# Kernel tuning notes

Hardware: AMD Instinct MI355X
Metric: run time of the kernel (lower is better)

## Reference

```python
import jax, jax.numpy as jnp
import numpy as np

B, S, D, V, ML = 8, 1024, 768, 32000, 2000
EPS = 1e-5


def layernorm(x, g, b):
    mu = jnp.mean(x, axis=-1, keepdims=True)
    var = jnp.mean(jnp.square(x - mu), axis=-1, keepdims=True)
    return (x - mu) * jax.lax.rsqrt(var + EPS) * g + b


def setup_inputs() -> dict:
    key = jax.random.key(0)
    ks = jax.random.split(key, 16)
    idx = jax.random.randint(ks[0], (B, S), 0, V)
    attention_mask = jax.random.randint(ks[1], (B, S), 0, 2).astype(jnp.int32)
    # guarantee at least one valid key per row so softmax rows are finite
    attention_mask = attention_mask.at[:, 0].set(1)
    s = 0.02
    return {
        "idx": idx,
        "attention_mask": attention_mask,
        "emb": jax.random.normal(ks[2], (V, D), jnp.float32) * s,
        "pos_emb": jax.random.normal(ks[3], (ML, D), jnp.float32) * s,
        "Wq": jax.random.normal(ks[4], (D, D), jnp.float32) * s,
        "Wk": jax.random.normal(ks[5], (D, D), jnp.float32) * s,
        "Wv": jax.random.normal(ks[6], (D, D), jnp.float32) * s,
        "ln1_g": jnp.ones((D,), jnp.float32),
        "ln1_b": jnp.zeros((D,), jnp.float32),
        "W1": jax.random.normal(ks[7], (D, D), jnp.float32) * s,
        "b1": jnp.zeros((D,), jnp.float32),
        "W2": jax.random.normal(ks[8], (D, D), jnp.float32) * s,
        "b2": jnp.zeros((D,), jnp.float32),
        "ln2_g": jnp.ones((D,), jnp.float32),
        "ln2_b": jnp.zeros((D,), jnp.float32),
    }


def reference(idx, attention_mask, emb, pos_emb, Wq, Wk, Wv, ln1_g, ln1_b,
              W1, b1, W2, b2, ln2_g, ln2_b):
    seq_len = idx.shape[1]
    x = emb[idx] + pos_emb[:seq_len]                       # [B,S,D]
    q = x @ Wq                                             # [B,S,D]
    k = x @ Wk
    v = x @ Wv
    att = jnp.einsum('bqd,bkd->bqk', q, k) * (D ** -0.5)   # [B,S,S]
    att = jnp.where(attention_mask[:, None, :] == 0, -jnp.inf, att)
    a = jax.nn.softmax(att, axis=-1) @ v                   # [B,S,D]
    x = layernorm(a, ln1_g, ln1_b)
    h = jax.nn.gelu(x @ W1 + b1, approximate=False)        # exact GELU (torch default)
    h = jax.nn.gelu(h @ W2 + b2, approximate=False)
    return layernorm(h, ln2_g, ln2_b)
```

## Files before the change

### kernel.cpp

```cpp
#include <hip/hip_runtime.h>
#include <hip/hip_bf16.h>
#include <math.h>

typedef __bf16 bf16;
typedef __attribute__((ext_vector_type(8))) __bf16 bf16x8;
typedef __attribute__((ext_vector_type(4))) __bf16 bf16x4;
typedef __attribute__((ext_vector_type(4))) float f32x4;

#define NB 8
#define SEQ 1024
#define DIM 768
#define ROWS (NB*SEQ)

__device__ __forceinline__ float gelu_exact(float x){
  return 0.5f * x * (1.0f + erff(x * 0.70710678118654752440f));
}

__device__ __forceinline__ void gload_lds16(const void* g, void* l){
  __builtin_amdgcn_global_load_lds((const __attribute__((address_space(1))) void*)g,
                                   (__attribute__((address_space(3))) void*)l, 16, 0, 0);
}

__global__ __launch_bounds__(192)
void k_embed(const int* __restrict__ idx, const float* __restrict__ emb,
             const float* __restrict__ pos, bf16* __restrict__ xo){
  const int row = blockIdx.x;
  const int s = row & (SEQ-1);
  const int tok = idx[row];
  const float* e = emb + (long)tok*DIM;
  const float* p = pos + (long)s*DIM;
  bf16* o = xo + (long)row*DIM;
  const int tid = threadIdx.x;
  f32x4 ev = *(const f32x4*)(e + tid*4);
  f32x4 pv = *(const f32x4*)(p + tid*4);
  bf16x4 ov;
  ov[0]=(bf16)(ev[0]+pv[0]); ov[1]=(bf16)(ev[1]+pv[1]);
  ov[2]=(bf16)(ev[2]+pv[2]); ov[3]=(bf16)(ev[3]+pv[3]);
  *(bf16x4*)(o + tid*4) = ov;
}

__global__ __launch_bounds__(256)
void k_transpose_bf16(const float* __restrict__ src, bf16* __restrict__ dst,
                      int K, int N){
  __shared__ float t[32][33];
  const int n0 = blockIdx.x*32, k0 = blockIdx.y*32;
  const int tx = threadIdx.x, ty = threadIdx.y;
  #pragma unroll
  for (int i=0;i<4;i++)
    t[ty+i*8][tx] = src[(long)(k0+ty+i*8)*N + n0 + tx];
  __syncthreads();
  #pragma unroll
  for (int i=0;i<4;i++)
    dst[(long)(n0+ty+i*8)*K + k0 + tx] = (bf16)t[tx][ty+i*8];
}

__global__ __launch_bounds__(256)
void k_transpose_v(const bf16* __restrict__ qkv, bf16* __restrict__ vT){
  __shared__ bf16 t[32][33];
  const int b = blockIdx.z;
  const int s0 = blockIdx.x*32, d0 = blockIdx.y*32;
  const int tx = threadIdx.x, ty = threadIdx.y;
  const bf16* src = qkv + (long)b*SEQ*2304 + 1536;
  bf16* dst = vT + (long)b*DIM*SEQ;
  #pragma unroll
  for (int i=0;i<4;i++)
    t[ty+i*8][tx] = src[(long)(s0+ty+i*8)*2304 + d0 + tx];
  __syncthreads();
  #pragma unroll
  for (int i=0;i<4;i++)
    dst[(long)(d0+ty+i*8)*SEQ + s0 + tx] = t[tx][ty+i*8];
}

template<int EPI>
__global__ __launch_bounds__(512, 2)
void k_gemm(const bf16* __restrict__ A, int lda, long sA,
            const bf16* __restrict__ Bt, int ldb, long sB,
            void* __restrict__ Cv, int ldc, long sC,
            int K,
            const float* __restrict__ bias,
            const int* __restrict__ mask, int maskStride,
            float scale, int swizzle)
{
  __shared__ __align__(16) bf16 As[2][256][64];
  __shared__ __align__(16) bf16 Bs[2][256][64];

  const int bz = blockIdx.z;
  A  += (long)bz * sA;
  Bt += (long)bz * sB;

  int bx = blockIdx.x, by = blockIdx.y;
  if (swizzle){
    const int gx = gridDim.x;
    const int T  = gx * gridDim.y;
    const int flat = by*gx + bx;
    const int logical = (flat & 7)*(T>>3) + (flat>>3);
    bx = logical % gx;
    by = logical / gx;
  }
  const int m0 = bx*256, n0 = by*256;

  const int tid  = threadIdx.x;
  const int lane = tid & 63;
  const int w    = tid >> 6;
  const int wm   = w >> 2;
  const int wn   = w & 3;
  const int hb   = wn >> 1;
  const int gb   = wm*2 + (wn & 1);
  const int ga   = wn;

  const int l8    = lane >> 3;
  const int lslot = (lane & 7) ^ l8;

  const bf16* Agbase = A  + (long)(m0 + wm*128)*lda + lslot*8;
  const bf16* Bgbase = Bt + (long)(n0 + hb*128)*ldb + lslot*8;

  auto stageA = [&](int buf, int kt, int c){
    const bf16* g = Agbase + (long)(c*8 + l8)*lda + kt*64;
    char* l = (char*)&As[buf][0][0] + wm*16384 + c*1024;
    gload_lds16(g, l);
  };
  auto stageB = [&](int buf, int kt, int c){
    const bf16* g = Bgbase + (long)(c*8 + l8)*ldb + kt*64;
    char* l = (char*)&Bs[buf][0][0] + hb*16384 + c*1024;
    gload_lds16(g, l);
  };
  auto ldsA = [&](int buf, int mf, int ks)->bf16x8 {
    const int row  = wm*128 + mf*16 + (lane & 15);
    const int slot = (ks*4 + (lane>>4)) ^ (row & 7);
    return *(const bf16x8*)((const char*)&As[buf][0][0] + row*128 + slot*16);
  };
  auto ldsB = [&](int buf, int nf, int ks)->bf16x8 {
    const int row  = wn*64 + nf*16 + (lane & 15);
    const int slot = (ks*4 + (lane>>4)) ^ (row & 7);
    return *(const bf16x8*)((const char*)&Bs[buf][0][0] + row*128 + slot*16);
  };

  f32x4 acc[8][4];
  const f32x4 zero = {0.f,0.f,0.f,0.f};
  #pragma unroll
  for (int i=0;i<8;i++)
    #pragma unroll
    for (int j=0;j<4;j++) acc[i][j] = zero;

  bf16x8 bfr[4][2];
  const int nk = K >> 6;

  stageB(0,0, gb);    stageB(0,0, gb+4);
  stageB(0,0, gb+8);  stageB(0,0, gb+12);
  stageA(0,0, ga);    stageA(0,0, ga+4);
  stageA(0,0, ga+8);  stageA(0,0, ga+12);
  asm volatile("s_waitcnt vmcnt(2)\ns_barrier" ::: "memory");

  for (int t=0; t<nk; ++t){
    const int buf = t & 1;
    const bool st = (t+1 < nk);
    #pragma unroll
    for (int q=0; q<4; ++q){
      bf16x8 afr[2][2];
      #pragma unroll
      for (int i=0;i<2;i++)
        #pragma unroll
        for (int ks=0;ks<2;ks++)
          afr[i][ks] = ldsA(buf, 2*q+i, ks);
      if (q==0){
        #pragma unroll
        for (int nf=0;nf<4;nf++)
          #pragma unroll
          for (int ks=0;ks<2;ks++)
            bfr[nf][ks] = ldsB(buf, nf, ks);
      }
      if (st){
        if (q==0){ stageB(buf^1, t+1, gb);    stageB(buf^1, t+1, gb+4);  }
        if (q==1){ stageB(buf^1, t+1, gb+8);  stageB(buf^1, t+1, gb+12); }
        if (q==2){ stageA(buf^1, t+1, ga);    stageA(buf^1, t+1, ga+4);  }
        if (q==3){ stageA(buf^1, t+1, ga+8);  stageA(buf^1, t+1, ga+12); }
      }
      if (st){
        if (q==3) asm volatile("s_waitcnt vmcnt(2)\ns_barrier" ::: "memory");
        else      asm volatile("s_waitcnt vmcnt(4)\ns_barrier" ::: "memory");
      } else {
        if (q==1) asm volatile("s_waitcnt vmcnt(0)\ns_barrier" ::: "memory");
        else      asm volatile("s_barrier" ::: "memory");
      }
      __builtin_amdgcn_s_setprio(1);
      #pragma unroll
      for (int i=0;i<2;i++)
        #pragma unroll
        for (int nf=0;nf<4;nf++)
          #pragma unroll
          for (int ks=0;ks<2;ks++)
            acc[2*q+i][nf] = __builtin_amdgcn_mfma_f32_16x16x32_bf16(
                afr[i][ks], bfr[nf][ks], acc[2*q+i][nf], 0, 0, 0);
      __builtin_amdgcn_s_setprio(0);
      asm volatile("s_barrier" ::: "memory");
    }
  }

  const int cm0 = m0 + wm*128 + ((lane>>4)<<2);
  const int cn0 = n0 + wn*64  + (lane & 15);
  const long cb = (long)bz * sC;
  const int* mk = (EPI==3) ? (mask + (long)bz*maskStride) : nullptr;

  #pragma unroll
  for (int mf=0; mf<8; mf++){
    #pragma unroll
    for (int nf=0; nf<4; nf++){
      #pragma unroll
      for (int r=0; r<4; r++){
        const int m = cm0 + mf*16 + r;
        const int n = cn0 + nf*16;
        const long o = cb + (long)m*ldc + n;
        float c = acc[mf][nf][r];
        if (EPI == 0){
          ((bf16*)Cv)[o] = (bf16)c;
        } else if (EPI == 1){
          ((bf16*)Cv)[o] = (bf16)gelu_exact(c + bias[n]);
        } else if (EPI == 2){
          ((float*)Cv)[o] = gelu_exact(c + bias[n]);
        } else if (EPI == 3){
          ((float*)Cv)[o] = (mk[n] != 0) ? c*scale : -1e30f;
        } else {
          ((float*)Cv)[o] = c;
        }
      }
    }
  }
}

__global__ __launch_bounds__(256)
void k_softmax(const float* __restrict__ att, bf16* __restrict__ P){
  __shared__ float red[4];
  __shared__ float red2[4];
  const int row = blockIdx.x;
  const float* a = att + (long)row * SEQ;
  bf16* p = P + (long)row * SEQ;
  const int tid = threadIdx.x;
  f32x4 v = *(const f32x4*)(a + tid*4);
  float m = fmaxf(fmaxf(v[0],v[1]), fmaxf(v[2],v[3]));
  #pragma unroll
  for (int o=32;o>0;o>>=1) m = fmaxf(m, __shfl_xor(m, o));
  if ((tid&63)==0) red[tid>>6] = m;
  __syncthreads();
  m = fmaxf(fmaxf(red[0],red[1]), fmaxf(red[2],red[3]));
  float e0 = expf(v[0]-m), e1 = expf(v[1]-m), e2 = expf(v[2]-m), e3 = expf(v[3]-m);
  float s = e0+e1+e2+e3;
  #pragma unroll
  for (int o=32;o>0;o>>=1) s += __shfl_xor(s, o);
  if ((tid&63)==0) red2[tid>>6] = s;
  __syncthreads();
  s = red2[0]+red2[1]+red2[2]+red2[3];
  const float inv = 1.0f / s;
  bf16x4 pw;
  pw[0]=(bf16)(e0*inv); pw[1]=(bf16)(e1*inv); pw[2]=(bf16)(e2*inv); pw[3]=(bf16)(e3*inv);
  *(bf16x4*)(p + tid*4) = pw;
}

template<int OUT_BF16>
__global__ __launch_bounds__(256)
void k_layernorm(const float* __restrict__ X, const float* __restrict__ g,
                 const float* __restrict__ b, void* __restrict__ Yv){
  __shared__ float red[4];
  __shared__ float red2[4];
  const int row = blockIdx.x;
  const float* x = X + (long)row*DIM;
  const int tid = threadIdx.x;
  float v0=x[tid], v1=x[tid+256], v2=x[tid+512];
  float s = v0+v1+v2;
  #pragma unroll
  for (int o=32;o>0;o>>=1) s += __shfl_xor(s, o);
  if ((tid&63)==0) red[tid>>6] = s;
  __syncthreads();
  s = red[0]+red[1]+red[2]+red[3];
  const float mu = s * (1.0f/768.0f);
  const float d0=v0-mu, d1=v1-mu, d2=v2-mu;
  float q = d0*d0+d1*d1+d2*d2;
  #pragma unroll
  for (int o=32;o>0;o>>=1) q += __shfl_xor(q, o);
  if ((tid&63)==0) red2[tid>>6] = q;
  __syncthreads();
  q = red2[0]+red2[1]+red2[2]+red2[3];
  const float r = rsqrtf(q*(1.0f/768.0f) + 1e-5f);
  const float y0 = d0*r*g[tid]     + b[tid];
  const float y1 = d1*r*g[tid+256] + b[tid+256];
  const float y2 = d2*r*g[tid+512] + b[tid+512];
  if (OUT_BF16){
    bf16* Y = (bf16*)Yv;
    Y[(long)row*DIM+tid]=(bf16)y0; Y[(long)row*DIM+tid+256]=(bf16)y1; Y[(long)row*DIM+tid+512]=(bf16)y2;
  } else {
    float* Y = (float*)Yv;
    Y[(long)row*DIM+tid]=y0; Y[(long)row*DIM+tid+256]=y1; Y[(long)row*DIM+tid+512]=y2;
  }
}

extern "C" void kernel_launch(void* const* d_in, const int* in_sizes, int n_in,
                              void* d_out, int out_size, void* d_ws, size_t ws_size,
                              hipStream_t stream)
{
  (void)in_sizes; (void)n_in; (void)out_size; (void)ws_size;
  const int*   idx  = (const int*)d_in[0];
  const int*   am   = (const int*)d_in[1];
  const float* emb  = (const float*)d_in[2];
  const float* pos  = (const float*)d_in[3];
  const float* Wq   = (const float*)d_in[4];
  const float* Wk   = (const float*)d_in[5];
  const float* Wv   = (const float*)d_in[6];
  const float* ln1g = (const float*)d_in[7];
  const float* ln1b = (const float*)d_in[8];
  const float* W1   = (const float*)d_in[9];
  const float* b1   = (const float*)d_in[10];
  const float* W2   = (const float*)d_in[11];
  const float* b2   = (const float*)d_in[12];
  const float* ln2g = (const float*)d_in[13];
  const float* ln2b = (const float*)d_in[14];

  char* ws = (char*)d_ws;
  size_t off = 0;
  auto take = [&](size_t bytes)->char*{
    char* p = ws + off;
    off += (bytes + 255) & ~(size_t)255;
    return p;
  };
  bf16*  Wqkvt = (bf16*) take((size_t)2304*768*2);
  bf16*  W1t   = (bf16*) take((size_t)768*768*2);
  bf16*  W2t   = (bf16*) take((size_t)768*768*2);
  bf16*  xbf   = (bf16*) take((size_t)ROWS*DIM*2);
  bf16*  qkv   = (bf16*) take((size_t)ROWS*2304*2);
  bf16*  vT    = (bf16*) take((size_t)NB*DIM*SEQ*2);
  float* att   = (float*)take((size_t)NB*SEQ*SEQ*4);
  bf16*  P     = (bf16*) take((size_t)NB*SEQ*SEQ*2);
  float* aout  = (float*)take((size_t)ROWS*DIM*4);
  bf16*  x1    = (bf16*) take((size_t)ROWS*DIM*2);
  bf16*  h1    = (bf16*) take((size_t)ROWS*DIM*2);
  float* h2    = (float*)take((size_t)ROWS*DIM*4);
  float* out   = (float*)d_out;

  const dim3 tb(32,8);
  const dim3 tg(24,24);
  k_transpose_bf16<<<tg, tb, 0, stream>>>(Wq, Wqkvt,            768, 768);
  k_transpose_bf16<<<tg, tb, 0, stream>>>(Wk, Wqkvt + 768*768,  768, 768);
  k_transpose_bf16<<<tg, tb, 0, stream>>>(Wv, Wqkvt + 1536*768, 768, 768);
  k_transpose_bf16<<<tg, tb, 0, stream>>>(W1, W1t, 768, 768);
  k_transpose_bf16<<<tg, tb, 0, stream>>>(W2, W2t, 768, 768);

  k_embed<<<ROWS, 192, 0, stream>>>(idx, emb, pos, xbf);

  k_gemm<0><<<dim3(32,9,1), 512, 0, stream>>>(xbf,768,0L, Wqkvt,768,0L,
                                              qkv,2304,0L, 768,
                                              nullptr, nullptr,0, 1.0f, 1);

  k_transpose_v<<<dim3(32,24,8), tb, 0, stream>>>(qkv, vT);

  k_gemm<3><<<dim3(4,4,8), 512, 0, stream>>>(
      qkv,     2304, (long)SEQ*2304,
      qkv+768, 2304, (long)SEQ*2304,
      att,     SEQ,  (long)SEQ*SEQ,
      768, nullptr, am, SEQ, 0.03608439182435161f, 0);

  k_softmax<<<ROWS, 256, 0, stream>>>(att, P);

  k_gemm<4><<<dim3(4,3,8), 512, 0, stream>>>(
      P,    SEQ, (long)SEQ*SEQ,
      vT,   SEQ, (long)DIM*SEQ,
      aout, DIM, (long)SEQ*DIM,
      1024, nullptr, nullptr,0, 1.0f, 0);

  k_layernorm<1><<<ROWS, 256, 0, stream>>>(aout, ln1g, ln1b, x1);

  k_gemm<1><<<dim3(32,3,1), 512, 0, stream>>>(x1,768,0L, W1t,768,0L, h1,768,0L,
                                              768, b1, nullptr,0, 1.0f, 1);
  k_gemm<2><<<dim3(32,3,1), 512, 0, stream>>>(h1,768,0L, W2t,768,0L, h2,768,0L,
                                              768, b2, nullptr,0, 1.0f, 1);

  k_layernorm<0><<<ROWS, 256, 0, stream>>>(h2, ln2g, ln2b, out);
}
```

Measured before the change: 403.8 us.

## Add smaller-tile GEMM for attention/MLP, store scores in bf16, merge weight transposes

Adds a 128x128 tile, 256-thread double-buffered GEMM and uses it for QK^T, PV and both MLP GEMMs. The QKV projection keeps the large 256x256 tile kernel. The goal is more blocks on undersized grids such as 4x4x8 and 4x3x8, which should fill more compute units. Attention scores are now written and read as bf16 instead of fp32, halving that traffic at some cost in precision. The five weight-transpose launches become one launch.

```diff
diff --git a/kernel.cpp b/kernel.cpp
--- a/kernel.cpp
+++ b/kernel.cpp
@@ -40,18 +40,23 @@
 }
 
 __global__ __launch_bounds__(256)
-void k_transpose_bf16(const float* __restrict__ src, bf16* __restrict__ dst,
-                      int K, int N){
+void k_transpose_w(const float* __restrict__ Wq, const float* __restrict__ Wk,
+                   const float* __restrict__ Wv, const float* __restrict__ W1,
+                   const float* __restrict__ W2,
+                   bf16* __restrict__ Wqkvt, bf16* __restrict__ W1t, bf16* __restrict__ W2t){
   __shared__ float t[32][33];
+  const int z = blockIdx.z;
+  const float* src = (z==0)?Wq:(z==1)?Wk:(z==2)?Wv:(z==3)?W1:W2;
+  bf16* dst = (z<3) ? (Wqkvt + (size_t)z*768*768) : ((z==3)?W1t:W2t);
   const int n0 = blockIdx.x*32, k0 = blockIdx.y*32;
   const int tx = threadIdx.x, ty = threadIdx.y;
   #pragma unroll
   for (int i=0;i<4;i++)
-    t[ty+i*8][tx] = src[(long)(k0+ty+i*8)*N + n0 + tx];
+    t[ty+i*8][tx] = src[(long)(k0+ty+i*8)*768 + n0 + tx];
   __syncthreads();
   #pragma unroll
   for (int i=0;i<4;i++)
-    dst[(long)(n0+ty+i*8)*K + k0 + tx] = (bf16)t[tx][ty+i*8];
+    dst[(long)(n0+ty+i*8)*768 + k0 + tx] = (bf16)t[tx][ty+i*8];
 }
 
 __global__ __launch_bounds__(256)
@@ -72,14 +77,118 @@
 }
 
 template<int EPI>
+__global__ __launch_bounds__(256, 2)
+void k_gemm2p(const bf16* __restrict__ A, int lda, long sA,
+              const bf16* __restrict__ Bt, int ldb, long sB,
+              void* __restrict__ Cv, int ldc, long sC,
+              int K,
+              const float* __restrict__ bias,
+              const int* __restrict__ mask, int maskStride,
+              float scale)
+{
+  __shared__ __align__(16) bf16 As[2][128][32];
+  __shared__ __align__(16) bf16 Bs[2][128][32];
+
+  const int bz = blockIdx.z;
+  A  += (long)bz * sA;
+  Bt += (long)bz * sB;
+  const int m0 = blockIdx.x * 128;
+  const int n0 = blockIdx.y * 128;
+
+  const int tid  = threadIdx.x;
+  const int lane = tid & 63;
+  const int w    = tid >> 6;
+
+  const int st_row = w*16 + (lane>>2);
+  const int st_col = (lane&3)*8;
+  const bf16* Ag0 = A  + (long)(m0 + st_row)*lda + st_col;
+  const bf16* Bg0 = Bt + (long)(n0 + st_row)*ldb + st_col;
+
+  const int nk = K >> 5;
+
+  f32x4 acc[4][4];
+  const f32x4 zero = {0.f,0.f,0.f,0.f};
+  #pragma unroll
+  for (int i=0;i<4;i++)
+    #pragma unroll
+    for (int j=0;j<4;j++) acc[i][j] = zero;
+
+  const int wr = (w>>1)*64;
+  const int wc = (w&1)*64;
+  const int fr = lane & 15;
+  const int fk = (lane>>4)*8;
+
+  {
+    char* lA = (char*)&As[0][0][0] + w*1024;
+    char* lB = (char*)&Bs[0][0][0] + w*1024;
+    gload_lds16(Ag0,                lA);
+    gload_lds16(Ag0 + (long)64*lda, lA + 4096);
+    gload_lds16(Bg0,                lB);
+    gload_lds16(Bg0 + (long)64*ldb, lB + 4096);
+  }
+
+  int buf = 0;
+  for (int kt=0; kt<nk; kt++){
+    __syncthreads();
+    if (kt+1 < nk){
+      const bf16* Ag = Ag0 + (kt+1)*32;
+      const bf16* Bg = Bg0 + (kt+1)*32;
+      char* lA = (char*)&As[buf^1][0][0] + w*1024;
+      char* lB = (char*)&Bs[buf^1][0][0] + w*1024;
+      gload_lds16(Ag,                lA);
+      gload_lds16(Ag + (long)64*lda, lA + 4096);
+      gload_lds16(Bg,                lB);
+      gload_lds16(Bg + (long)64*ldb, lB + 4096);
+    }
+    bf16x8 af[4], bfv[4];
+    #pragma unroll
+    for (int t=0;t<4;t++){
+      af[t]  = *(const bf16x8*)&As[buf][wr + t*16 + fr][fk];
+      bfv[t] = *(const bf16x8*)&Bs[buf][wc + t*16 + fr][fk];
+    }
+    #pragma unroll
+    for (int mt=0;mt<4;mt++)
+      #pragma unroll
+      for (int nt=0;nt<4;nt++)
+        acc[mt][nt] = __builtin_amdgcn_mfma_f32_16x16x32_bf16(af[mt], bfv[nt], acc[mt][nt], 0, 0, 0);
+    buf ^= 1;
+  }
+
+  const int cm0 = m0 + wr + ((lane>>4)<<2);
+  const int cn0 = n0 + wc + fr;
+  const long cb = (long)bz * sC;
+  const int* mk = (EPI==3) ? (mask + (long)bz*maskStride) : nullptr;
+
+  #pragma unroll
+  for (int mt=0;mt<4;mt++){
+    #pragma unroll
+    for (int nt=0;nt<4;nt++){
+      #pragma unroll
+      for (int r=0;r<4;r++){
+        const int m = cm0 + mt*16 + r;
+        const int n = cn0 + nt*16;
+        const long o = cb + (long)m*ldc + n;
+        float c = acc[mt][nt][r];
+        if (EPI == 1){
+          ((bf16*)Cv)[o] = (bf16)gelu_exact(c + bias[n]);
+        } else if (EPI == 2){
+          ((float*)Cv)[o] = gelu_exact(c + bias[n]);
+        } else if (EPI == 3){
+          ((bf16*)Cv)[o] = (bf16)((mk[n] != 0) ? c*scale : -1e30f);
+        } else {
+          ((float*)Cv)[o] = c;
+        }
+      }
+    }
+  }
+}
+
+template<int EPI>
 __global__ __launch_bounds__(512, 2)
-void k_gemm(const bf16* __restrict__ A, int lda, long sA,
-            const bf16* __restrict__ Bt, int ldb, long sB,
-            void* __restrict__ Cv, int ldc, long sC,
-            int K,
-            const float* __restrict__ bias,
-            const int* __restrict__ mask, int maskStride,
-            float scale, int swizzle)
+void k_gemm4p(const bf16* __restrict__ A, int lda, long sA,
+              const bf16* __restrict__ Bt, int ldb, long sB,
+              void* __restrict__ Cv, int ldc, long sC,
+              int K, int swizzle)
 {
   __shared__ __align__(16) bf16 As[2][256][64];
   __shared__ __align__(16) bf16 Bs[2][256][64];
@@ -199,7 +308,6 @@
   const int cm0 = m0 + wm*128 + ((lane>>4)<<2);
   const int cn0 = n0 + wn*64  + (lane & 15);
   const long cb = (long)bz * sC;
-  const int* mk = (EPI==3) ? (mask + (long)bz*maskStride) : nullptr;
 
   #pragma unroll
   for (int mf=0; mf<8; mf++){
@@ -210,39 +318,29 @@
         const int m = cm0 + mf*16 + r;
         const int n = cn0 + nf*16;
         const long o = cb + (long)m*ldc + n;
-        float c = acc[mf][nf][r];
-        if (EPI == 0){
-          ((bf16*)Cv)[o] = (bf16)c;
-        } else if (EPI == 1){
-          ((bf16*)Cv)[o] = (bf16)gelu_exact(c + bias[n]);
-        } else if (EPI == 2){
-          ((float*)Cv)[o] = gelu_exact(c + bias[n]);
-        } else if (EPI == 3){
-          ((float*)Cv)[o] = (mk[n] != 0) ? c*scale : -1e30f;
-        } else {
-          ((float*)Cv)[o] = c;
-        }
+        ((bf16*)Cv)[o] = (bf16)acc[mf][nf][r];
       }
     }
   }
 }
 
 __global__ __launch_bounds__(256)
-void k_softmax(const float* __restrict__ att, bf16* __restrict__ P){
+void k_softmax(const bf16* __restrict__ att, bf16* __restrict__ P){
   __shared__ float red[4];
   __shared__ float red2[4];
   const int row = blockIdx.x;
-  const float* a = att + (long)row * SEQ;
+  const bf16* a = att + (long)row * SEQ;
   bf16* p = P + (long)row * SEQ;
   const int tid = threadIdx.x;
-  f32x4 v = *(const f32x4*)(a + tid*4);
-  float m = fmaxf(fmaxf(v[0],v[1]), fmaxf(v[2],v[3]));
+  bf16x4 v4 = *(const bf16x4*)(a + tid*4);
+  float v0=(float)v4[0], v1=(float)v4[1], v2=(float)v4[2], v3=(float)v4[3];
+  float m = fmaxf(fmaxf(v0,v1), fmaxf(v2,v3));
   #pragma unroll
   for (int o=32;o>0;o>>=1) m = fmaxf(m, __shfl_xor(m, o));
   if ((tid&63)==0) red[tid>>6] = m;
   __syncthreads();
   m = fmaxf(fmaxf(red[0],red[1]), fmaxf(red[2],red[3]));
-  float e0 = expf(v[0]-m), e1 = expf(v[1]-m), e2 = expf(v[2]-m), e3 = expf(v[3]-m);
+  float e0 = expf(v0-m), e1 = expf(v1-m), e2 = expf(v2-m), e3 = expf(v3-m);
   float s = e0+e1+e2+e3;
   #pragma unroll
   for (int o=32;o>0;o>>=1) s += __shfl_xor(s, o);
@@ -326,7 +424,7 @@
   bf16*  xbf   = (bf16*) take((size_t)ROWS*DIM*2);
   bf16*  qkv   = (bf16*) take((size_t)ROWS*2304*2);
   bf16*  vT    = (bf16*) take((size_t)NB*DIM*SEQ*2);
-  float* att   = (float*)take((size_t)NB*SEQ*SEQ*4);
+  bf16*  att   = (bf16*) take((size_t)NB*SEQ*SEQ*2);
   bf16*  P     = (bf16*) take((size_t)NB*SEQ*SEQ*2);
   float* aout  = (float*)take((size_t)ROWS*DIM*4);
   bf16*  x1    = (bf16*) take((size_t)ROWS*DIM*2);
@@ -334,42 +432,35 @@
   float* h2    = (float*)take((size_t)ROWS*DIM*4);
   float* out   = (float*)d_out;
 
-  const dim3 tb(32,8);
-  const dim3 tg(24,24);
-  k_transpose_bf16<<<tg, tb, 0, stream>>>(Wq, Wqkvt,            768, 768);
-  k_transpose_bf16<<<tg, tb, 0, stream>>>(Wk, Wqkvt + 768*768,  768, 768);
-  k_transpose_bf16<<<tg, tb, 0, stream>>>(Wv, Wqkvt + 1536*768, 768, 768);
-  k_transpose_bf16<<<tg, tb, 0, stream>>>(W1, W1t, 768, 768);
-  k_transpose_bf16<<<tg, tb, 0, stream>>>(W2, W2t, 768, 768);
+  k_transpose_w<<<dim3(24,24,5), dim3(32,8), 0, stream>>>(Wq,Wk,Wv,W1,W2, Wqkvt,W1t,W2t);
 
   k_embed<<<ROWS, 192, 0, stream>>>(idx, emb, pos, xbf);
 
-  k_gemm<0><<<dim3(32,9,1), 512, 0, stream>>>(xbf,768,0L, Wqkvt,768,0L,
-                                              qkv,2304,0L, 768,
-                                              nullptr, nullptr,0, 1.0f, 1);
-
-  k_transpose_v<<<dim3(32,24,8), tb, 0, stream>>>(qkv, vT);
-
-  k_gemm<3><<<dim3(4,4,8), 512, 0, stream>>>(
+  k_gemm4p<0><<<dim3(32,9,1), 512, 0, stream>>>(xbf,768,0L, Wqkvt,768,0L,
+                                                qkv,2304,0L, 768, 1);
+
+  k_transpose_v<<<dim3(32,24,8), dim3(32,8), 0, stream>>>(qkv, vT);
+
+  k_gemm2p<3><<<dim3(8,8,8), 256, 0, stream>>>(
       qkv,     2304, (long)SEQ*2304,
       qkv+768, 2304, (long)SEQ*2304,
       att,     SEQ,  (long)SEQ*SEQ,
-      768, nullptr, am, SEQ, 0.03608439182435161f, 0);
+      768, nullptr, am, SEQ, 0.03608439182435161f);
 
   k_softmax<<<ROWS, 256, 0, stream>>>(att, P);
 
-  k_gemm<4><<<dim3(4,3,8), 512, 0, stream>>>(
+  k_gemm2p<4><<<dim3(8,6,8), 256, 0, stream>>>(
       P,    SEQ, (long)SEQ*SEQ,
       vT,   SEQ, (long)DIM*SEQ,
       aout, DIM, (long)SEQ*DIM,
-      1024, nullptr, nullptr,0, 1.0f, 0);
+      1024, nullptr, nullptr,0, 1.0f);
 
   k_layernorm<1><<<ROWS, 256, 0, stream>>>(aout, ln1g, ln1b, x1);
 
-  k_gemm<1><<<dim3(32,3,1), 512, 0, stream>>>(x1,768,0L, W1t,768,0L, h1,768,0L,
-                                              768, b1, nullptr,0, 1.0f, 1);
-  k_gemm<2><<<dim3(32,3,1), 512, 0, stream>>>(h1,768,0L, W2t,768,0L, h2,768,0L,
-                                              768, b2, nullptr,0, 1.0f, 1);
+  k_gemm2p<1><<<dim3(64,6,1), 256, 0, stream>>>(x1,768,0L, W1t,768,0L, h1,768,0L,
+                                                768, b1, nullptr,0, 1.0f);
+  k_gemm2p<2><<<dim3(64,6,1), 256, 0, stream>>>(h1,768,0L, W2t,768,0L, h2,768,0L,
+                                                768, b2, nullptr,0, 1.0f);
 
   k_layernorm<0><<<ROWS, 256, 0, stream>>>(h2, ln2g, ln2b, out);
 }
```

Measured after the change: 378.0 us. 6.4% less time.
